# Kernel optimization log

Measured on AMD Instinct MI355X. Metric: run time of the kernel, lower is better.

The kernel has to match this reference:

```python
import jax, jax.numpy as jnp
import numpy as np

NUM_GRAPHS = 128


def _gcn_conv(x, W, b, src, dst, norm, n_nodes):
    # PyG GCNConv: linear transform, then symmetric-normalized scatter-add aggregation
    h = x @ W                                  # [N, out]
    msg = norm[:, None] * h[src]               # [E+N, out] gathered messages
    out = jax.ops.segment_sum(msg, dst, num_segments=n_nodes)
    return out + b


def setup_inputs() -> dict:
    key = jax.random.key(0)
    ks = jax.random.split(key, 12)
    N, E, H, GE, C = 100000, 1000000, 64, 64, 5
    x = jax.random.normal(ks[0], (N, 2), dtype=jnp.float32)
    edge_index = jax.random.randint(ks[1], (2, E), 0, N, dtype=jnp.int32)
    batch = jnp.sort(jax.random.randint(ks[2], (N,), 0, NUM_GRAPHS, dtype=jnp.int32))
    graph_embedding = jax.random.normal(ks[3], (NUM_GRAPHS, GE), dtype=jnp.float32)
    s = lambda k, shape, fan: jax.random.normal(k, shape, dtype=jnp.float32) * (1.0 / np.sqrt(fan))
    W1 = s(ks[4], (2, H), 2); b1 = jnp.zeros((H,), jnp.float32)
    W2 = s(ks[5], (H, H), H); b2 = jnp.zeros((H,), jnp.float32)
    W3 = s(ks[6], (H, H), H); b3 = jnp.zeros((H,), jnp.float32)
    Wl = s(ks[7], (H + GE, C), H + GE); bl = jnp.zeros((C,), jnp.float32)
    return {"x": x, "edge_index": edge_index, "batch": batch,
            "graph_embedding": graph_embedding,
            "W1": W1, "b1": b1, "W2": W2, "b2": b2, "W3": W3, "b3": b3,
            "Wl": Wl, "bl": bl}


def reference(x, edge_index, batch, graph_embedding, W1, b1, W2, b2, W3, b3, Wl, bl):
    N = x.shape[0]
    loops = jnp.arange(N, dtype=edge_index.dtype)
    src = jnp.concatenate([edge_index[0], loops])   # add self-loops
    dst = jnp.concatenate([edge_index[1], loops])
    deg = jax.ops.segment_sum(jnp.ones_like(dst, dtype=x.dtype), dst, num_segments=N)
    dinv = jnp.where(deg > 0, jax.lax.rsqrt(deg), 0.0)
    norm = dinv[src] * dinv[dst]                    # [E+N]

    h = jax.nn.relu(_gcn_conv(x, W1, b1, src, dst, norm, N))
    h = jax.nn.relu(_gcn_conv(h, W2, b2, src, dst, norm, N))
    h = _gcn_conv(h, W3, b3, src, dst, norm, N)

    # global mean pool over graphs
    sums = jax.ops.segment_sum(h, batch, num_segments=NUM_GRAPHS)
    cnts = jax.ops.segment_sum(jnp.ones((N,), x.dtype), batch, num_segments=NUM_GRAPHS)
    pooled = sums / jnp.maximum(cnts, 1.0)[:, None]

    z = jnp.concatenate([pooled, graph_embedding], axis=1) @ Wl + bl
    return jax.nn.log_softmax(z, axis=1)
```

## Files before the change

kernel.cpp:

```cpp
#include <hip/hip_runtime.h>
#include <hip/hip_bf16.h>
#include <math.h>

#define NG 128
#define CHUNKB 4096
#define NBIN 512
#define EWIN 256
#define STAGE_CAP 6144

typedef __attribute__((ext_vector_type(8))) short short8;
typedef __attribute__((ext_vector_type(4))) float float4v;
typedef __attribute__((ext_vector_type(4))) uint uint4v;

__global__ void k_bin_hist(const int* __restrict__ dst, int* __restrict__ hist,
                           int e, int nb, float* __restrict__ sums,
                           const float* __restrict__ W2, const float* __restrict__ W3,
                           __hip_bfloat16* __restrict__ Wf2, __hip_bfloat16* __restrict__ Wf3) {
    __shared__ int h[NBIN];
    int blk = blockIdx.x;
    if (blk >= nb) {
        int ex = blk - nb;
        if (ex == 0) {
            for (int i = threadIdx.x; i < NG * 64; i += 256) sums[i] = 0.0f;
        } else {
            const float* W = (ex == 2) ? W3 : W2;
            __hip_bfloat16* Wf = (ex == 2) ? Wf3 : Wf2;
            for (int t = threadIdx.x; t < 512; t += 256) {
                int c = t >> 6, l = t & 63;
                int jt = c >> 1, half = c & 1, nn = l & 15, q = l >> 4;
                #pragma unroll
                for (int j = 0; j < 8; j++) {
                    int k = half * 32 + q * 8 + j;
                    Wf[t * 8 + j] = __float2bfloat16(W[k * 64 + jt * 16 + nn]);
                }
            }
        }
        return;
    }
    for (int i = threadIdx.x; i < NBIN; i += 256) h[i] = 0;
    __syncthreads();
    int base = blk * CHUNKB;
    int lim = e - base; if (lim > CHUNKB) lim = CHUNKB;
    for (int k = threadIdx.x; k < lim; k += 256)
        atomicAdd(&h[dst[base + k] >> 8], 1);
    __syncthreads();
    for (int b = threadIdx.x; b < NBIN; b += 256) hist[b * nb + blk] = h[b];
}

__global__ void __launch_bounds__(512) genscan1(int* __restrict__ a, int* __restrict__ bsums, int n) {
    __shared__ int s[512];
    int tid = threadIdx.x;
    int i = blockIdx.x * 512 + tid;
    int v = (i < n) ? a[i] : 0;
    s[tid] = v;
    __syncthreads();
    for (int d = 1; d < 512; d <<= 1) {
        int t = (tid >= d) ? s[tid - d] : 0;
        __syncthreads();
        s[tid] += t;
        __syncthreads();
    }
    if (i < n) a[i] = s[tid] - v;
    if (tid == 511) bsums[blockIdx.x] = s[511];
}

__global__ void __launch_bounds__(512) genscan2(int* __restrict__ bsums, int nb) {
    __shared__ int s[512];
    int tid = threadIdx.x;
    int v = (tid < nb) ? bsums[tid] : 0;
    s[tid] = v;
    __syncthreads();
    for (int d = 1; d < 512; d <<= 1) {
        int t = (tid >= d) ? s[tid - d] : 0;
        __syncthreads();
        s[tid] += t;
        __syncthreads();
    }
    if (tid < nb) bsums[tid] = s[tid] - v;
}

__global__ void k_bin_scatter(const int* __restrict__ srcs, const int* __restrict__ dsts,
                              const int* __restrict__ offsets, const int* __restrict__ bsums,
                              int2* __restrict__ outbuf, int e, int nb) {
    __shared__ int hcnt[NBIN];
    __shared__ int lstart[NBIN];
    __shared__ int ss[256];
    __shared__ int2 stage[CHUNKB];
    int tid = threadIdx.x, blk = blockIdx.x, base = blk * CHUNKB;
    int lim = e - base; if (lim > CHUNKB) lim = CHUNKB;
    for (int i = tid; i < NBIN; i += 256) hcnt[i] = 0;
    __syncthreads();
    for (int k = tid; k < lim; k += 256)
        atomicAdd(&hcnt[dsts[base + k] >> 8], 1);
    __syncthreads();
    int c0 = hcnt[2 * tid], c1 = hcnt[2 * tid + 1];
    int sum = c0 + c1;
    ss[tid] = sum;
    __syncthreads();
    for (int d = 1; d < 256; d <<= 1) {
        int t = (tid >= d) ? ss[tid - d] : 0;
        __syncthreads();
        ss[tid] += t;
        __syncthreads();
    }
    int excl = ss[tid] - sum;
    lstart[2 * tid] = excl;
    lstart[2 * tid + 1] = excl + c0;
    __syncthreads();
    hcnt[2 * tid] = excl;
    hcnt[2 * tid + 1] = excl + c0;
    __syncthreads();
    for (int k = tid; k < lim; k += 256) {
        int2 ed = make_int2(srcs[base + k], dsts[base + k]);
        int p = atomicAdd(&hcnt[ed.y >> 8], 1);
        stage[p] = ed;
    }
    __syncthreads();
    for (int i = tid; i < NBIN; i += 256) {
        int gi = i * nb + blk;
        lstart[i] = offsets[gi] + bsums[gi >> 9] - lstart[i];
    }
    __syncthreads();
    for (int p = tid; p < lim; p += 256) {
        int2 ed = stage[p];
        outbuf[lstart[ed.y >> 8] + p] = ed;
    }
}

__global__ void k_csrAB(const int2* __restrict__ ebuck, const int* __restrict__ offsets,
                        const int* __restrict__ bsums, const float* __restrict__ x,
                        int* __restrict__ row_ptr, float* __restrict__ dinv,
                        float2* __restrict__ xs, int* __restrict__ csr,
                        int n, int nb, int e_total) {
    __shared__ int lcnt[256];
    __shared__ int ssc[256];
    __shared__ int rstart[256];
    __shared__ int2 stage[STAGE_CAP];
    int b = blockIdx.x, tid = threadIdx.x, n0 = b << 8;
    lcnt[tid] = 0;
    __syncthreads();
    int i0 = b * nb, i1 = (b + 1) * nb;
    int e0 = offsets[i0] + bsums[i0 >> 9];
    int e1 = offsets[i1] + bsums[i1 >> 9];
    int cnt = e1 - e0;
    bool fast = (cnt <= STAGE_CAP);
    if (fast) {
        for (int i = e0 + tid; i < e1; i += 256) {
            int2 ed = ebuck[i];
            stage[i - e0] = ed;
            atomicAdd(&lcnt[ed.y - n0], 1);
        }
    } else {
        for (int i = e0 + tid; i < e1; i += 256)
            atomicAdd(&lcnt[ebuck[i].y - n0], 1);
    }
    __syncthreads();
    int v = lcnt[tid];
    ssc[tid] = v;
    __syncthreads();
    for (int d = 1; d < 256; d <<= 1) {
        int t = (tid >= d) ? ssc[tid - d] : 0;
        __syncthreads();
        ssc[tid] += t;
        __syncthreads();
    }
    int rs = e0 + ssc[tid] - v;
    rstart[tid] = rs;
    int node = n0 + tid;
    if (node < n) {
        row_ptr[node] = rs;
        float dv = rsqrtf((float)v + 1.0f);
        dinv[node] = dv;
        const float2* x2 = (const float2*)x;
        float2 xi = x2[node];
        xs[node] = make_float2(xi.x * dv, xi.y * dv);
        if (node == n - 1) row_ptr[n] = e_total;
    }
    lcnt[tid] = 0;
    __syncthreads();
    if (fast) {
        for (int i = tid; i < cnt; i += 256) {
            int2 ed = stage[i];
            int li = ed.y - n0;
            int r = atomicAdd(&lcnt[li], 1);
            csr[rstart[li] + r] = ed.x;
        }
    } else {
        for (int i = e0 + tid; i < e1; i += 256) {
            int2 ed = ebuck[i];
            int li = ed.y - n0;
            int r = atomicAdd(&lcnt[li], 1);
            csr[rstart[li] + r] = ed.x;
        }
    }
}

__global__ void k_layer1(const int* __restrict__ row_ptr, const int* __restrict__ edges,
                         const float2* __restrict__ xs, const float* __restrict__ dinv,
                         const float* __restrict__ W1, const float* __restrict__ b1,
                         __hip_bfloat16* __restrict__ h, int n) {
    __shared__ float w1s[128];
    __shared__ float b1s[64];
    if (threadIdx.x < 128) w1s[threadIdx.x] = W1[threadIdx.x];
    if (threadIdx.x < 64) b1s[threadIdx.x] = b1[threadIdx.x];
    __syncthreads();
    int i = blockIdx.x * blockDim.x + threadIdx.x;
    if (i >= n) return;
    float dd = dinv[i];
    float2 xi = xs[i];
    float a0 = xi.x, a1 = xi.y;
    int lo = row_ptr[i], hi = row_ptr[i + 1];
    int k = lo;
    for (; k + 4 <= hi; k += 4) {
        int s0 = edges[k], s1 = edges[k + 1], s2 = edges[k + 2], s3 = edges[k + 3];
        float2 v0 = xs[s0], v1 = xs[s1], v2 = xs[s2], v3 = xs[s3];
        a0 += v0.x + v1.x + v2.x + v3.x;
        a1 += v0.y + v1.y + v2.y + v3.y;
    }
    for (; k < hi; k++) {
        float2 v = xs[edges[k]];
        a0 += v.x;
        a1 += v.y;
    }
    a0 *= dd; a1 *= dd;
    short8* hv = reinterpret_cast<short8*>(h + (size_t)i * 64);
    #pragma unroll
    for (int g = 0; g < 8; g++) {
        short8 pack;
        #pragma unroll
        for (int j = 0; j < 8; j++) {
            int col = g * 8 + j;
            float v = fmaxf(a0 * w1s[col] + a1 * w1s[64 + col] + b1s[col], 0.0f);
            v *= dd;
            __hip_bfloat16 bv = __float2bfloat16(v);
            pack[j] = *reinterpret_cast<short*>(&bv);
        }
        hv[g] = pack;
    }
}

static __device__ __forceinline__ void acc8(float* a, uint4v v) {
    #pragma unroll
    for (int i = 0; i < 4; i++) {
        uint u = v[i];
        a[2 * i]     += __int_as_float(u << 16);
        a[2 * i + 1] += __int_as_float(u & 0xffff0000u);
    }
}

template <bool FAST>
static __device__ __forceinline__ void agg_group(int lo, int cnt, int mc, int c,
        const int* __restrict__ gE, const int* EW, int wave_lo,
        const uint4v* __restrict__ hin4, float* acc) {
    for (int j = 0; j < mc; j += 2) {
        bool ok0 = j < cnt, ok1 = j + 1 < cnt;
        int e0 = ok0 ? lo + j : wave_lo;
        int e1 = ok1 ? lo + j + 1 : wave_lo;
        int s0 = FAST ? EW[e0 - wave_lo] : gE[e0];
        int s1 = FAST ? EW[e1 - wave_lo] : gE[e1];
        uint4v v0 = hin4[(size_t)s0 * 8 + c];
        uint4v v1 = hin4[(size_t)s1 * 8 + c];
        if (!ok0) v0 = (uint4v){0u, 0u, 0u, 0u};
        if (!ok1) v1 = (uint4v){0u, 0u, 0u, 0u};
        acc8(acc, v0);
        acc8(acc, v1);
    }
}

template <int RELU, int POOL>
__global__ void __launch_bounds__(64, 8) k_aggLin(const int* __restrict__ row_ptr,
                                                  const int* __restrict__ edges,
                                                  const __hip_bfloat16* __restrict__ hin,
                                                  const float* __restrict__ dinv,
                                                  const __hip_bfloat16* __restrict__ Wf,
                                                  const float* __restrict__ b,
                                                  __hip_bfloat16* __restrict__ hout,
                                                  const int* __restrict__ batch,
                                                  float* __restrict__ sums, int n) {
    __shared__ __attribute__((aligned(16))) __hip_bfloat16 T[16 * 72];
    __shared__ int EW[EWIN];
    int lane = threadIdx.x;
    int nb0 = blockIdx.x * 16;
    if (nb0 >= n) return;
    int g = lane >> 3;
    int c = lane & 7;
    const uint4v* hin4 = reinterpret_cast<const uint4v*>(hin);

    int bidx = nb0 + (lane < 16 ? lane : 16);
    if (bidx > n) bidx = n;
    int rp = row_ptr[bidx];
    int wave_lo = __shfl(rp, 0);
    int wave_hi = __shfl(rp, 16);
    int cnt_all = wave_hi - wave_lo;
    bool fast = (cnt_all <= EWIN);
    if (fast)
        for (int i = lane; i < cnt_all; i += 64) EW[i] = edges[wave_lo + i];

    #pragma unroll
    for (int h8 = 0; h8 < 2; h8++) {
        int nn = h8 * 8 + g;
        int node = nb0 + nn;
        float acc[8] = {0.f, 0.f, 0.f, 0.f, 0.f, 0.f, 0.f, 0.f};
        int lo = __shfl(rp, nn);
        int hi = __shfl(rp, nn + 1);
        int cnt = (node < n) ? (hi - lo) : 0;
        int mc = cnt;
        mc = max(mc, __shfl_xor(mc, 8));
        mc = max(mc, __shfl_xor(mc, 16));
        mc = max(mc, __shfl_xor(mc, 32));
        if (node < n)
            acc8(acc, hin4[(size_t)node * 8 + c]);
        if (fast) agg_group<true >(lo, cnt, mc, c, edges, EW, wave_lo, hin4, acc);
        else      agg_group<false>(lo, cnt, mc, c, edges, EW, wave_lo, hin4, acc);
        float dv = (node < n) ? dinv[node] : 0.0f;
        uint4v pk;
        #pragma unroll
        for (int i = 0; i < 4; i++) {
            __hip_bfloat16 bx = __float2bfloat16(acc[2 * i] * dv);
            __hip_bfloat16 by = __float2bfloat16(acc[2 * i + 1] * dv);
            pk[i] = (uint)(*reinterpret_cast<unsigned short*>(&bx)) |
                    ((uint)(*reinterpret_cast<unsigned short*>(&by)) << 16);
        }
        *reinterpret_cast<uint4v*>(&T[nn * 72 + c * 8]) = pk;
    }

    int m = lane & 15, q = lane >> 4;
    short8 a0 = *reinterpret_cast<const short8*>(&T[m * 72 + q * 8]);
    short8 a1 = *reinterpret_cast<const short8*>(&T[m * 72 + 32 + q * 8]);
    int lastn = nb0 + 15 < n ? nb0 + 15 : n - 1;
    bool onegraph = POOL && (nb0 + 15 < n) && (batch[nb0] == batch[lastn]);
    int gA = POOL ? batch[nb0] : 0;
    float dvs[4];
    if (!POOL) {
        #pragma unroll
        for (int r = 0; r < 4; r++) {
            int node = nb0 + q * 4 + r;
            dvs[r] = node < n ? dinv[node] : 0.0f;
        }
    }
    #pragma unroll
    for (int jt = 0; jt < 4; jt++) {
        short8 bf0 = *reinterpret_cast<const short8*>(Wf + ((size_t)(jt * 2 + 0) * 64 + lane) * 8);
        short8 bf1 = *reinterpret_cast<const short8*>(Wf + ((size_t)(jt * 2 + 1) * 64 + lane) * 8);
        float4v d = {0.0f, 0.0f, 0.0f, 0.0f};
        d = __builtin_amdgcn_mfma_f32_16x16x32_bf16(a0, bf0, d, 0, 0, 0);
        d = __builtin_amdgcn_mfma_f32_16x16x32_bf16(a1, bf1, d, 0, 0, 0);
        float bias = b[jt * 16 + m];
        if (POOL) {
            if (onegraph) {
                float s = (d[0] + bias) + (d[1] + bias) + (d[2] + bias) + (d[3] + bias);
                s += __shfl_xor(s, 16);
                s += __shfl_xor(s, 32);
                if (q == 0) atomicAdd(&sums[gA * 64 + jt * 16 + m], s);
            } else {
                #pragma unroll
                for (int r = 0; r < 4; r++) {
                    int node = nb0 + q * 4 + r;
                    if (node < n)
                        atomicAdd(&sums[batch[node] * 64 + jt * 16 + m], d[r] + bias);
                }
            }
        } else {
            #pragma unroll
            for (int r = 0; r < 4; r++) {
                int node = nb0 + q * 4 + r;
                if (node < n) {
                    float v = d[r] + bias;
                    if (RELU) v = fmaxf(v, 0.0f);
                    v *= dvs[r];
                    hout[(size_t)node * 64 + jt * 16 + m] = __float2bfloat16(v);
                }
            }
        }
    }
}

__device__ inline int lower_bound_i(const int* __restrict__ a, int n, int key) {
    int lo = 0, hi = n;
    while (lo < hi) {
        int mid = (lo + hi) >> 1;
        if (a[mid] < key) lo = mid + 1; else hi = mid;
    }
    return lo;
}

__global__ void k_head(const float* __restrict__ sums, const int* __restrict__ batch,
                       const float* __restrict__ ge, const float* __restrict__ Wl,
                       const float* __restrict__ bl, float* __restrict__ out,
                       int n, int ng) {
    int g = blockIdx.x * blockDim.x + threadIdx.x;
    if (g < ng) {
        int lo = lower_bound_i(batch, n, g);
        int hi = lower_bound_i(batch, n, g + 1);
        float c = fmaxf((float)(hi - lo), 1.0f);
        float z[5];
        for (int cl = 0; cl < 5; cl++) z[cl] = bl[cl];
        for (int k = 0; k < 64; k++) {
            float p = sums[g * 64 + k] / c;
            for (int cl = 0; cl < 5; cl++) z[cl] += p * Wl[k * 5 + cl];
        }
        for (int k = 0; k < 64; k++) {
            float p = ge[g * 64 + k];
            for (int cl = 0; cl < 5; cl++) z[cl] += p * Wl[(64 + k) * 5 + cl];
        }
        float m = z[0];
        for (int cl = 1; cl < 5; cl++) m = fmaxf(m, z[cl]);
        float s = 0.0f;
        for (int cl = 0; cl < 5; cl++) s += expf(z[cl] - m);
        float lse = m + logf(s);
        for (int cl = 0; cl < 5; cl++) out[g * 5 + cl] = z[cl] - lse;
    }
}

#define ALIGN16(x) (((x) + 15) & ~(size_t)15)

extern "C" void kernel_launch(void* const* d_in, const int* in_sizes, int n_in,
                              void* d_out, int out_size, void* d_ws, size_t ws_size,
                              hipStream_t stream) {
    const float* x    = (const float*)d_in[0];
    const int*   ei   = (const int*)d_in[1];
    const int*   batch= (const int*)d_in[2];
    const float* ge   = (const float*)d_in[3];
    const float* W1   = (const float*)d_in[4];
    const float* b1   = (const float*)d_in[5];
    const float* W2   = (const float*)d_in[6];
    const float* b2   = (const float*)d_in[7];
    const float* W3   = (const float*)d_in[8];
    const float* b3   = (const float*)d_in[9];
    const float* Wl   = (const float*)d_in[10];
    const float* bl   = (const float*)d_in[11];
    float* out = (float*)d_out;

    const int N = in_sizes[0] / 2;
    const int E = in_sizes[1] / 2;
    const int* src = ei;
    const int* dst = ei + E;
    const int NBUK = (N + 255) >> 8;
    const int nbC  = (E + CHUNKB - 1) / CHUNKB;

    char* wsb = (char*)d_ws;
    float* dinv   = (float*)wsb;                wsb += ALIGN16((size_t)N * 4);
    float2* xs    = (float2*)wsb;               wsb += ALIGN16((size_t)N * 8);
    __hip_bfloat16* h16 = (__hip_bfloat16*)wsb;  wsb += ALIGN16((size_t)64 * N * 2);
    __hip_bfloat16* buf2= (__hip_bfloat16*)wsb;  wsb += ALIGN16((size_t)64 * N * 2);
    float* sums   = (float*)wsb;                wsb += ALIGN16((size_t)NG * 64 * 4);
    __hip_bfloat16* Wf2 = (__hip_bfloat16*)wsb; wsb += ALIGN16((size_t)4096 * 2);
    __hip_bfloat16* Wf3 = (__hip_bfloat16*)wsb; wsb += ALIGN16((size_t)4096 * 2);
    int2*  ebuck  = (int2*)wsb;                 wsb += ALIGN16((size_t)E * 8);
    int*   csr    = (int*)wsb;                  wsb += ALIGN16((size_t)E * 4);
    int*   row_ptr= (int*)wsb;                  wsb += ALIGN16((size_t)(N + 1) * 4);
    int*   hist   = (int*)wsb;                  wsb += ALIGN16((size_t)NBIN * nbC * 4);
    int*   bsums  = (int*)wsb;                  wsb += 512 * 4;

    const int BS = 256;
    int gN   = (N + BS - 1) / BS;
    int gF   = (N + 15) / 16;
    int nH   = NBIN * nbC;
    int gH   = (nH + 511) / 512;

    k_bin_hist<<<nbC + 3, BS, 0, stream>>>(dst, hist, E, nbC, sums, W2, W3, Wf2, Wf3);
    genscan1<<<gH, 512, 0, stream>>>(hist, bsums, nH);
    genscan2<<<1, 512, 0, stream>>>(bsums, gH);
    k_bin_scatter<<<nbC, BS, 0, stream>>>(src, dst, hist, bsums, ebuck, E, nbC);
    k_csrAB<<<NBUK, BS, 0, stream>>>(ebuck, hist, bsums, x, row_ptr, dinv, xs, csr,
                                     N, nbC, E);

    k_layer1<<<gN, BS, 0, stream>>>(row_ptr, csr, xs, dinv, W1, b1, h16, N);

    k_aggLin<1, 0><<<gF, 64, 0, stream>>>(row_ptr, csr, h16, dinv, Wf2, b2, buf2,
                                          nullptr, nullptr, N);

    k_aggLin<0, 1><<<gF, 64, 0, stream>>>(row_ptr, csr, buf2, dinv, Wf3, b3, nullptr,
                                          batch, sums, N);

    k_head<<<1, 128, 0, stream>>>(sums, batch, ge, Wl, bl, out, N, NG);
}
```

Baseline: 199.7 us.

## Pack edge buckets into 32-bit, widen aggregation blocks, fuse head into last layer

Edge bucketing now packs the destination's low 8 bits with the 24-bit source into one int, which halves the bucket buffer traffic, and the scatter chunk size is halved to 2048. The aggregation kernel runs four waves per 256-thread block. Each lane interleaves two nodes' gathers, and padded rows use a zero sentinel row at index N in place of masking. The separate head kernel is removed and folded into the final layer with a last-block ticket counter, which saves one launch. The packing assumes fewer than 2^24 nodes, and the ticket adds fence and serialization overhead in the last block.

```diff
diff --git a/kernel.cpp b/kernel.cpp
--- a/kernel.cpp
+++ b/kernel.cpp
@@ -3,9 +3,10 @@
 #include <math.h>
 
 #define NG 128
-#define CHUNKB 4096
+#define CHUNKB 2048
 #define NBIN 512
-#define EWIN 256
+#define EWIN 320
+#define EWPAD 384
 #define STAGE_CAP 6144
 
 typedef __attribute__((ext_vector_type(8))) short short8;
@@ -15,13 +16,19 @@
 __global__ void k_bin_hist(const int* __restrict__ dst, int* __restrict__ hist,
                            int e, int nb, float* __restrict__ sums,
                            const float* __restrict__ W2, const float* __restrict__ W3,
-                           __hip_bfloat16* __restrict__ Wf2, __hip_bfloat16* __restrict__ Wf3) {
+                           __hip_bfloat16* __restrict__ Wf2, __hip_bfloat16* __restrict__ Wf3,
+                           __hip_bfloat16* __restrict__ h16, __hip_bfloat16* __restrict__ buf2,
+                           int* __restrict__ ticket, int n) {
     __shared__ int h[NBIN];
     int blk = blockIdx.x;
     if (blk >= nb) {
         int ex = blk - nb;
         if (ex == 0) {
             for (int i = threadIdx.x; i < NG * 64; i += 256) sums[i] = 0.0f;
+            if (threadIdx.x == 0) *ticket = 0;
+            uint* hz = (uint*)(h16 + (size_t)n * 64);
+            uint* bz = (uint*)(buf2 + (size_t)n * 64);
+            if (threadIdx.x < 32) { hz[threadIdx.x] = 0u; bz[threadIdx.x] = 0u; }
         } else {
             const float* W = (ex == 2) ? W3 : W2;
             __hip_bfloat16* Wf = (ex == 2) ? Wf3 : Wf2;
@@ -81,11 +88,12 @@
 
 __global__ void k_bin_scatter(const int* __restrict__ srcs, const int* __restrict__ dsts,
                               const int* __restrict__ offsets, const int* __restrict__ bsums,
-                              int2* __restrict__ outbuf, int e, int nb) {
+                              int* __restrict__ outbuf, int e, int nb) {
     __shared__ int hcnt[NBIN];
     __shared__ int lstart[NBIN];
     __shared__ int ss[256];
-    __shared__ int2 stage[CHUNKB];
+    __shared__ int stage[CHUNKB];
+    __shared__ int sbuck[CHUNKB];
     int tid = threadIdx.x, blk = blockIdx.x, base = blk * CHUNKB;
     int lim = e - base; if (lim > CHUNKB) lim = CHUNKB;
     for (int i = tid; i < NBIN; i += 256) hcnt[i] = 0;
@@ -111,9 +119,11 @@
     hcnt[2 * tid + 1] = excl + c0;
     __syncthreads();
     for (int k = tid; k < lim; k += 256) {
-        int2 ed = make_int2(srcs[base + k], dsts[base + k]);
-        int p = atomicAdd(&hcnt[ed.y >> 8], 1);
-        stage[p] = ed;
+        int s = srcs[base + k], d = dsts[base + k];
+        int bk = d >> 8;
+        int p = atomicAdd(&hcnt[bk], 1);
+        stage[p] = ((d & 255) << 24) | s;
+        sbuck[p] = bk;
     }
     __syncthreads();
     for (int i = tid; i < NBIN; i += 256) {
@@ -121,13 +131,11 @@
         lstart[i] = offsets[gi] + bsums[gi >> 9] - lstart[i];
     }
     __syncthreads();
-    for (int p = tid; p < lim; p += 256) {
-        int2 ed = stage[p];
-        outbuf[lstart[ed.y >> 8] + p] = ed;
-    }
-}
-
-__global__ void k_csrAB(const int2* __restrict__ ebuck, const int* __restrict__ offsets,
+    for (int p = tid; p < lim; p += 256)
+        outbuf[lstart[sbuck[p]] + p] = stage[p];
+}
+
+__global__ void k_csrAB(const int* __restrict__ ebuck, const int* __restrict__ offsets,
                         const int* __restrict__ bsums, const float* __restrict__ x,
                         int* __restrict__ row_ptr, float* __restrict__ dinv,
                         float2* __restrict__ xs, int* __restrict__ csr,
@@ -135,7 +143,7 @@
     __shared__ int lcnt[256];
     __shared__ int ssc[256];
     __shared__ int rstart[256];
-    __shared__ int2 stage[STAGE_CAP];
+    __shared__ int stage[STAGE_CAP];
     int b = blockIdx.x, tid = threadIdx.x, n0 = b << 8;
     lcnt[tid] = 0;
     __syncthreads();
@@ -146,13 +154,13 @@
     bool fast = (cnt <= STAGE_CAP);
     if (fast) {
         for (int i = e0 + tid; i < e1; i += 256) {
-            int2 ed = ebuck[i];
-            stage[i - e0] = ed;
-            atomicAdd(&lcnt[ed.y - n0], 1);
+            int p = ebuck[i];
+            stage[i - e0] = p;
+            atomicAdd(&lcnt[(uint)p >> 24], 1);
         }
     } else {
         for (int i = e0 + tid; i < e1; i += 256)
-            atomicAdd(&lcnt[ebuck[i].y - n0], 1);
+            atomicAdd(&lcnt[(uint)ebuck[i] >> 24], 1);
     }
     __syncthreads();
     int v = lcnt[tid];
@@ -180,17 +188,17 @@
     __syncthreads();
     if (fast) {
         for (int i = tid; i < cnt; i += 256) {
-            int2 ed = stage[i];
-            int li = ed.y - n0;
+            int p = stage[i];
+            int li = (uint)p >> 24;
             int r = atomicAdd(&lcnt[li], 1);
-            csr[rstart[li] + r] = ed.x;
+            csr[rstart[li] + r] = p & 0xFFFFFF;
         }
     } else {
         for (int i = e0 + tid; i < e1; i += 256) {
-            int2 ed = ebuck[i];
-            int li = ed.y - n0;
+            int p = ebuck[i];
+            int li = (uint)p >> 24;
             int r = atomicAdd(&lcnt[li], 1);
-            csr[rstart[li] + r] = ed.x;
+            csr[rstart[li] + r] = p & 0xFFFFFF;
         }
     }
 }
@@ -248,167 +256,183 @@
     }
 }
 
-template <bool FAST>
-static __device__ __forceinline__ void agg_group(int lo, int cnt, int mc, int c,
-        const int* __restrict__ gE, const int* EW, int wave_lo,
-        const uint4v* __restrict__ hin4, float* acc) {
-    for (int j = 0; j < mc; j += 2) {
-        bool ok0 = j < cnt, ok1 = j + 1 < cnt;
-        int e0 = ok0 ? lo + j : wave_lo;
-        int e1 = ok1 ? lo + j + 1 : wave_lo;
-        int s0 = FAST ? EW[e0 - wave_lo] : gE[e0];
-        int s1 = FAST ? EW[e1 - wave_lo] : gE[e1];
-        uint4v v0 = hin4[(size_t)s0 * 8 + c];
-        uint4v v1 = hin4[(size_t)s1 * 8 + c];
-        if (!ok0) v0 = (uint4v){0u, 0u, 0u, 0u};
-        if (!ok1) v1 = (uint4v){0u, 0u, 0u, 0u};
-        acc8(acc, v0);
-        acc8(acc, v1);
-    }
-}
-
 template <int RELU, int POOL>
-__global__ void __launch_bounds__(64, 8) k_aggLin(const int* __restrict__ row_ptr,
-                                                  const int* __restrict__ edges,
-                                                  const __hip_bfloat16* __restrict__ hin,
-                                                  const float* __restrict__ dinv,
-                                                  const __hip_bfloat16* __restrict__ Wf,
-                                                  const float* __restrict__ b,
-                                                  __hip_bfloat16* __restrict__ hout,
-                                                  const int* __restrict__ batch,
-                                                  float* __restrict__ sums, int n) {
-    __shared__ __attribute__((aligned(16))) __hip_bfloat16 T[16 * 72];
-    __shared__ int EW[EWIN];
-    int lane = threadIdx.x;
-    int nb0 = blockIdx.x * 16;
-    if (nb0 >= n) return;
-    int g = lane >> 3;
-    int c = lane & 7;
-    const uint4v* hin4 = reinterpret_cast<const uint4v*>(hin);
-
-    int bidx = nb0 + (lane < 16 ? lane : 16);
-    if (bidx > n) bidx = n;
-    int rp = row_ptr[bidx];
-    int wave_lo = __shfl(rp, 0);
-    int wave_hi = __shfl(rp, 16);
-    int cnt_all = wave_hi - wave_lo;
-    bool fast = (cnt_all <= EWIN);
-    if (fast)
-        for (int i = lane; i < cnt_all; i += 64) EW[i] = edges[wave_lo + i];
-
-    #pragma unroll
-    for (int h8 = 0; h8 < 2; h8++) {
-        int nn = h8 * 8 + g;
-        int node = nb0 + nn;
-        float acc[8] = {0.f, 0.f, 0.f, 0.f, 0.f, 0.f, 0.f, 0.f};
-        int lo = __shfl(rp, nn);
-        int hi = __shfl(rp, nn + 1);
-        int cnt = (node < n) ? (hi - lo) : 0;
-        int mc = cnt;
-        mc = max(mc, __shfl_xor(mc, 8));
-        mc = max(mc, __shfl_xor(mc, 16));
-        mc = max(mc, __shfl_xor(mc, 32));
-        if (node < n)
-            acc8(acc, hin4[(size_t)node * 8 + c]);
-        if (fast) agg_group<true >(lo, cnt, mc, c, edges, EW, wave_lo, hin4, acc);
-        else      agg_group<false>(lo, cnt, mc, c, edges, EW, wave_lo, hin4, acc);
-        float dv = (node < n) ? dinv[node] : 0.0f;
-        uint4v pk;
+__global__ void __launch_bounds__(256, 6) k_aggLin(
+        const int* __restrict__ row_ptr, const int* __restrict__ edges,
+        const __hip_bfloat16* __restrict__ hin, const float* __restrict__ dinv,
+        const __hip_bfloat16* __restrict__ Wf, const float* __restrict__ b,
+        __hip_bfloat16* __restrict__ hout, const int* __restrict__ batch,
+        float* __restrict__ sums, int n,
+        const float* __restrict__ ge, const float* __restrict__ Wl,
+        const float* __restrict__ bl, float* __restrict__ out,
+        int* __restrict__ ticket) {
+    __shared__ __attribute__((aligned(16))) __hip_bfloat16 T[4][16 * 72];
+    __shared__ int EW[4][EWPAD];
+    __shared__ int lastflag;
+    int tid = threadIdx.x, wv = tid >> 6, lane = tid & 63;
+    int nb0 = blockIdx.x * 64 + wv * 16;
+    bool active = nb0 < n;
+    if (active) {
+        int g = lane >> 3, c = lane & 7;
+        const uint4v* hin4 = reinterpret_cast<const uint4v*>(hin);
+        int bidx = nb0 + (lane < 16 ? lane : 16);
+        if (bidx > n) bidx = n;
+        int rp = row_ptr[bidx];
+        int wave_lo = __shfl(rp, 0);
+        int wave_hi = __shfl(rp, 16);
+        int cnt_all = wave_hi - wave_lo;
+        int n0 = nb0 + g, n1 = nb0 + 8 + g;
+        int lo0 = __shfl(rp, g),     hi0 = __shfl(rp, g + 1);
+        int lo1 = __shfl(rp, 8 + g), hi1 = __shfl(rp, 9 + g);
+        int cnt0 = (n0 < n) ? hi0 - lo0 : 0;
+        int cnt1 = (n1 < n) ? hi1 - lo1 : 0;
+        int m01 = max(cnt0, cnt1);
+        m01 = max(m01, __shfl_xor(m01, 8));
+        m01 = max(m01, __shfl_xor(m01, 16));
+        m01 = max(m01, __shfl_xor(m01, 32));
+        bool fast = (cnt_all <= EWIN) && (m01 <= (EWPAD - EWIN));
+        int* ew = EW[wv];
+        if (fast)
+            for (int i = lane; i < cnt_all; i += 64) ew[i] = edges[wave_lo + i];
+        float acc0[8] = {0,0,0,0,0,0,0,0};
+        float acc1[8] = {0,0,0,0,0,0,0,0};
+        if (n0 < n) acc8(acc0, hin4[(size_t)n0 * 8 + c]);
+        if (n1 < n) acc8(acc1, hin4[(size_t)n1 * 8 + c]);
+        const int ZR = n;
+        if (fast) {
+            int o0 = lo0 - wave_lo, o1 = lo1 - wave_lo;
+            for (int j = 0; j < m01; j += 2) {
+                int sa = (j     < cnt0) ? ew[o0 + j]     : ZR;
+                int sb = (j + 1 < cnt0) ? ew[o0 + j + 1] : ZR;
+                int sc = (j     < cnt1) ? ew[o1 + j]     : ZR;
+                int sd = (j + 1 < cnt1) ? ew[o1 + j + 1] : ZR;
+                uint4v va = hin4[(size_t)sa * 8 + c];
+                uint4v vb = hin4[(size_t)sb * 8 + c];
+                uint4v vc = hin4[(size_t)sc * 8 + c];
+                uint4v vd = hin4[(size_t)sd * 8 + c];
+                acc8(acc0, va); acc8(acc0, vb);
+                acc8(acc1, vc); acc8(acc1, vd);
+            }
+        } else {
+            for (int j = 0; j < m01; j += 2) {
+                int ia = (j     < cnt0) ? lo0 + j     : wave_lo;
+                int ib = (j + 1 < cnt0) ? lo0 + j + 1 : wave_lo;
+                int ic = (j     < cnt1) ? lo1 + j     : wave_lo;
+                int id = (j + 1 < cnt1) ? lo1 + j + 1 : wave_lo;
+                int sa = edges[ia]; sa = (j     < cnt0) ? sa : ZR;
+                int sb = edges[ib]; sb = (j + 1 < cnt0) ? sb : ZR;
+                int sc = edges[ic]; sc = (j     < cnt1) ? sc : ZR;
+                int sd = edges[id]; sd = (j + 1 < cnt1) ? sd : ZR;
+                uint4v va = hin4[(size_t)sa * 8 + c];
+                uint4v vb = hin4[(size_t)sb * 8 + c];
+                uint4v vc = hin4[(size_t)sc * 8 + c];
+                uint4v vd = hin4[(size_t)sd * 8 + c];
+                acc8(acc0, va); acc8(acc0, vb);
+                acc8(acc1, vc); acc8(acc1, vd);
+            }
+        }
+        float dv0 = (n0 < n) ? dinv[n0] : 0.0f;
+        float dv1 = (n1 < n) ? dinv[n1] : 0.0f;
+        uint4v pk0, pk1;
         #pragma unroll
         for (int i = 0; i < 4; i++) {
-            __hip_bfloat16 bx = __float2bfloat16(acc[2 * i] * dv);
-            __hip_bfloat16 by = __float2bfloat16(acc[2 * i + 1] * dv);
-            pk[i] = (uint)(*reinterpret_cast<unsigned short*>(&bx)) |
-                    ((uint)(*reinterpret_cast<unsigned short*>(&by)) << 16);
-        }
-        *reinterpret_cast<uint4v*>(&T[nn * 72 + c * 8]) = pk;
-    }
-
-    int m = lane & 15, q = lane >> 4;
-    short8 a0 = *reinterpret_cast<const short8*>(&T[m * 72 + q * 8]);
-    short8 a1 = *reinterpret_cast<const short8*>(&T[m * 72 + 32 + q * 8]);
-    int lastn = nb0 + 15 < n ? nb0 + 15 : n - 1;
-    bool onegraph = POOL && (nb0 + 15 < n) && (batch[nb0] == batch[lastn]);
-    int gA = POOL ? batch[nb0] : 0;
-    float dvs[4];
-    if (!POOL) {
+            __hip_bfloat16 bx = __float2bfloat16(acc0[2 * i] * dv0);
+            __hip_bfloat16 by = __float2bfloat16(acc0[2 * i + 1] * dv0);
+            pk0[i] = (uint)(*reinterpret_cast<unsigned short*>(&bx)) |
+                     ((uint)(*reinterpret_cast<unsigned short*>(&by)) << 16);
+            __hip_bfloat16 cx = __float2bfloat16(acc1[2 * i] * dv1);
+            __hip_bfloat16 cy = __float2bfloat16(acc1[2 * i + 1] * dv1);
+            pk1[i] = (uint)(*reinterpret_cast<unsigned short*>(&cx)) |
+                     ((uint)(*reinterpret_cast<unsigned short*>(&cy)) << 16);
+        }
+        __hip_bfloat16* Tw = T[wv];
+        *reinterpret_cast<uint4v*>(&Tw[g * 72 + c * 8]) = pk0;
+        *reinterpret_cast<uint4v*>(&Tw[(8 + g) * 72 + c * 8]) = pk1;
+
+        int m = lane & 15, q = lane >> 4;
+        short8 a0 = *reinterpret_cast<const short8*>(&Tw[m * 72 + q * 8]);
+        short8 a1 = *reinterpret_cast<const short8*>(&Tw[m * 72 + 32 + q * 8]);
+        int lastn = nb0 + 15 < n ? nb0 + 15 : n - 1;
+        bool onegraph = POOL && (nb0 + 15 < n) && (batch[nb0] == batch[lastn]);
+        int gA = POOL ? batch[nb0] : 0;
+        float dvs[4];
+        if (!POOL) {
+            #pragma unroll
+            for (int r = 0; r < 4; r++) {
+                int node = nb0 + q * 4 + r;
+                dvs[r] = node < n ? dinv[node] : 0.0f;
+            }
+        }
         #pragma unroll
-        for (int r = 0; r < 4; r++) {
-            int node = nb0 + q * 4 + r;
-            dvs[r] = node < n ? dinv[node] : 0.0f;
-        }
-    }
-    #pragma unroll
-    for (int jt = 0; jt < 4; jt++) {
-        short8 bf0 = *reinterpret_cast<const short8*>(Wf + ((size_t)(jt * 2 + 0) * 64 + lane) * 8);
-        short8 bf1 = *reinterpret_cast<const short8*>(Wf + ((size_t)(jt * 2 + 1) * 64 + lane) * 8);
-        float4v d = {0.0f, 0.0f, 0.0f, 0.0f};
-        d = __builtin_amdgcn_mfma_f32_16x16x32_bf16(a0, bf0, d, 0, 0, 0);
-        d = __builtin_amdgcn_mfma_f32_16x16x32_bf16(a1, bf1, d, 0, 0, 0);
-        float bias = b[jt * 16 + m];
-        if (POOL) {
-            if (onegraph) {
-                float s = (d[0] + bias) + (d[1] + bias) + (d[2] + bias) + (d[3] + bias);
-                s += __shfl_xor(s, 16);
-                s += __shfl_xor(s, 32);
-                if (q == 0) atomicAdd(&sums[gA * 64 + jt * 16 + m], s);
+        for (int jt = 0; jt < 4; jt++) {
+            short8 bf0 = *reinterpret_cast<const short8*>(Wf + ((size_t)(jt * 2 + 0) * 64 + lane) * 8);
+            short8 bf1 = *reinterpret_cast<const short8*>(Wf + ((size_t)(jt * 2 + 1) * 64 + lane) * 8);
+            float4v d = {0.0f, 0.0f, 0.0f, 0.0f};
+            d = __builtin_amdgcn_mfma_f32_16x16x32_bf16(a0, bf0, d, 0, 0, 0);
+            d = __builtin_amdgcn_mfma_f32_16x16x32_bf16(a1, bf1, d, 0, 0, 0);
+            float bias = b[jt * 16 + m];
+            if (POOL) {
+                if (onegraph) {
+                    float s = (d[0] + bias) + (d[1] + bias) + (d[2] + bias) + (d[3] + bias);
+                    s += __shfl_xor(s, 16);
+                    s += __shfl_xor(s, 32);
+                    if (q == 0) atomicAdd(&sums[gA * 64 + jt * 16 + m], s);
+                } else {
+                    #pragma unroll
+                    for (int r = 0; r < 4; r++) {
+                        int node = nb0 + q * 4 + r;
+                        if (node < n)
+                            atomicAdd(&sums[batch[node] * 64 + jt * 16 + m], d[r] + bias);
+                    }
+                }
             } else {
                 #pragma unroll
                 for (int r = 0; r < 4; r++) {
                     int node = nb0 + q * 4 + r;
-                    if (node < n)
-                        atomicAdd(&sums[batch[node] * 64 + jt * 16 + m], d[r] + bias);
+                    if (node < n) {
+                        float v = d[r] + bias;
+                        if (RELU) v = fmaxf(v, 0.0f);
+                        v *= dvs[r];
+                        hout[(size_t)node * 64 + jt * 16 + m] = __float2bfloat16(v);
+                    }
                 }
             }
-        } else {
-            #pragma unroll
-            for (int r = 0; r < 4; r++) {
-                int node = nb0 + q * 4 + r;
-                if (node < n) {
-                    float v = d[r] + bias;
-                    if (RELU) v = fmaxf(v, 0.0f);
-                    v *= dvs[r];
-                    hout[(size_t)node * 64 + jt * 16 + m] = __float2bfloat16(v);
+        }
+    }
+    if (POOL) {
+        __threadfence();
+        __syncthreads();
+        if (tid == 0) {
+            int t = atomicAdd(ticket, 1);
+            lastflag = (t == (int)gridDim.x - 1);
+        }
+        __syncthreads();
+        if (lastflag) {
+            for (int gq = tid; gq < NG; gq += 256) {
+                int lo = 0, hi = n;
+                while (lo < hi) { int mid = (lo + hi) >> 1; if (batch[mid] < gq) lo = mid + 1; else hi = mid; }
+                int l0 = lo; lo = 0; hi = n;
+                while (lo < hi) { int mid = (lo + hi) >> 1; if (batch[mid] < gq + 1) lo = mid + 1; else hi = mid; }
+                float cdenom = fmaxf((float)(lo - l0), 1.0f);
+                float z[5];
+                for (int cl = 0; cl < 5; cl++) z[cl] = bl[cl];
+                for (int k = 0; k < 64; k++) {
+                    float p = __hip_atomic_load(&sums[gq * 64 + k], __ATOMIC_RELAXED,
+                                                __HIP_MEMORY_SCOPE_AGENT) / cdenom;
+                    for (int cl = 0; cl < 5; cl++) z[cl] += p * Wl[k * 5 + cl];
                 }
+                for (int k = 0; k < 64; k++) {
+                    float p = ge[gq * 64 + k];
+                    for (int cl = 0; cl < 5; cl++) z[cl] += p * Wl[(64 + k) * 5 + cl];
+                }
+                float mm = z[0];
+                for (int cl = 1; cl < 5; cl++) mm = fmaxf(mm, z[cl]);
+                float s = 0.0f;
+                for (int cl = 0; cl < 5; cl++) s += expf(z[cl] - mm);
+                float lse = mm + logf(s);
+                for (int cl = 0; cl < 5; cl++) out[gq * 5 + cl] = z[cl] - lse;
             }
         }
-    }
-}
-
-__device__ inline int lower_bound_i(const int* __restrict__ a, int n, int key) {
-    int lo = 0, hi = n;
-    while (lo < hi) {
-        int mid = (lo + hi) >> 1;
-        if (a[mid] < key) lo = mid + 1; else hi = mid;
-    }
-    return lo;
-}
-
-__global__ void k_head(const float* __restrict__ sums, const int* __restrict__ batch,
-                       const float* __restrict__ ge, const float* __restrict__ Wl,
-                       const float* __restrict__ bl, float* __restrict__ out,
-                       int n, int ng) {
-    int g = blockIdx.x * blockDim.x + threadIdx.x;
-    if (g < ng) {
-        int lo = lower_bound_i(batch, n, g);
-        int hi = lower_bound_i(batch, n, g + 1);
-        float c = fmaxf((float)(hi - lo), 1.0f);
-        float z[5];
-        for (int cl = 0; cl < 5; cl++) z[cl] = bl[cl];
-        for (int k = 0; k < 64; k++) {
-            float p = sums[g * 64 + k] / c;
-            for (int cl = 0; cl < 5; cl++) z[cl] += p * Wl[k * 5 + cl];
-        }
-        for (int k = 0; k < 64; k++) {
-            float p = ge[g * 64 + k];
-            for (int cl = 0; cl < 5; cl++) z[cl] += p * Wl[(64 + k) * 5 + cl];
-        }
-        float m = z[0];
-        for (int cl = 1; cl < 5; cl++) m = fmaxf(m, z[cl]);
-        float s = 0.0f;
-        for (int cl = 0; cl < 5; cl++) s += expf(z[cl] - m);
-        float lse = m + logf(s);
-        for (int cl = 0; cl < 5; cl++) out[g * 5 + cl] = z[cl] - lse;
     }
 }
 
@@ -441,24 +465,26 @@
     char* wsb = (char*)d_ws;
     float* dinv   = (float*)wsb;                wsb += ALIGN16((size_t)N * 4);
     float2* xs    = (float2*)wsb;               wsb += ALIGN16((size_t)N * 8);
-    __hip_bfloat16* h16 = (__hip_bfloat16*)wsb;  wsb += ALIGN16((size_t)64 * N * 2);
-    __hip_bfloat16* buf2= (__hip_bfloat16*)wsb;  wsb += ALIGN16((size_t)64 * N * 2);
+    __hip_bfloat16* h16 = (__hip_bfloat16*)wsb;  wsb += ALIGN16((size_t)64 * (N + 1) * 2);
+    __hip_bfloat16* buf2= (__hip_bfloat16*)wsb;  wsb += ALIGN16((size_t)64 * (N + 1) * 2);
     float* sums   = (float*)wsb;                wsb += ALIGN16((size_t)NG * 64 * 4);
     __hip_bfloat16* Wf2 = (__hip_bfloat16*)wsb; wsb += ALIGN16((size_t)4096 * 2);
     __hip_bfloat16* Wf3 = (__hip_bfloat16*)wsb; wsb += ALIGN16((size_t)4096 * 2);
-    int2*  ebuck  = (int2*)wsb;                 wsb += ALIGN16((size_t)E * 8);
+    int*   ebuck  = (int*)wsb;                  wsb += ALIGN16((size_t)E * 4);
     int*   csr    = (int*)wsb;                  wsb += ALIGN16((size_t)E * 4);
     int*   row_ptr= (int*)wsb;                  wsb += ALIGN16((size_t)(N + 1) * 4);
     int*   hist   = (int*)wsb;                  wsb += ALIGN16((size_t)NBIN * nbC * 4);
     int*   bsums  = (int*)wsb;                  wsb += 512 * 4;
+    int*   ticket = (int*)wsb;                  wsb += 16;
 
     const int BS = 256;
     int gN   = (N + BS - 1) / BS;
-    int gF   = (N + 15) / 16;
+    int gF4  = (N + 63) / 64;
     int nH   = NBIN * nbC;
     int gH   = (nH + 511) / 512;
 
-    k_bin_hist<<<nbC + 3, BS, 0, stream>>>(dst, hist, E, nbC, sums, W2, W3, Wf2, Wf3);
+    k_bin_hist<<<nbC + 3, BS, 0, stream>>>(dst, hist, E, nbC, sums, W2, W3, Wf2, Wf3,
+                                           h16, buf2, ticket, N);
     genscan1<<<gH, 512, 0, stream>>>(hist, bsums, nH);
     genscan2<<<1, 512, 0, stream>>>(bsums, gH);
     k_bin_scatter<<<nbC, BS, 0, stream>>>(src, dst, hist, bsums, ebuck, E, nbC);
@@ -467,11 +493,11 @@
 
     k_layer1<<<gN, BS, 0, stream>>>(row_ptr, csr, xs, dinv, W1, b1, h16, N);
 
-    k_aggLin<1, 0><<<gF, 64, 0, stream>>>(row_ptr, csr, h16, dinv, Wf2, b2, buf2,
-                                          nullptr, nullptr, N);
-
-    k_aggLin<0, 1><<<gF, 64, 0, stream>>>(row_ptr, csr, buf2, dinv, Wf3, b3, nullptr,
-                                          batch, sums, N);
-
-    k_head<<<1, 128, 0, stream>>>(sums, batch, ge, Wl, bl, out, N, NG);
-}
+    k_aggLin<1, 0><<<gF4, BS, 0, stream>>>(row_ptr, csr, h16, dinv, Wf2, b2, buf2,
+                                           nullptr, nullptr, N,
+                                           nullptr, nullptr, nullptr, nullptr, nullptr);
+
+    k_aggLin<0, 1><<<gF4, BS, 0, stream>>>(row_ptr, csr, buf2, dinv, Wf3, b3, nullptr,
+                                           batch, sums, N,
+                                           ge, Wl, bl, out, ticket);
+}
```

After: 297.2 us. 48.8% more time.
